# Performance work log

Measured on AMD Instinct MI355X. Metric: run time of the kernel, lower is better.

The kernel has to match this reference:

```python
import jax, jax.numpy as jnp
import numpy as np

N, E, F, HID, HEADS, G = 20000, 320000, 64, 64, 4, 64
HC = HEADS * HID  # 256
NHID, NOUT = 256, 128
INV_SQRT2 = 0.7071067811865476


def _gat(x, src, dst, W, a_s, a_d, bias):
    # GATConv (v1), eval mode (no dropout); src/dst already include self-loops (PyG default)
    H, C = a_s.shape
    h = (x @ W).reshape(-1, H, C)  # [N,H,C]
    al_s = jnp.einsum('nhc,hc->nh', h, a_s)
    al_d = jnp.einsum('nhc,hc->nh', h, a_d)
    e = jax.nn.leaky_relu(al_s[src] + al_d[dst], 0.2)  # [Etot,H]
    m = jax.ops.segment_max(e, dst, num_segments=N)
    ex = jnp.exp(e - m[dst])
    den = jax.ops.segment_sum(ex, dst, num_segments=N)
    coef = ex / den[dst]  # softmax over incoming edges per target node
    out = jax.ops.segment_sum(h[src] * coef[:, :, None], dst, num_segments=N)
    return out.reshape(-1, H * C) + bias


def _bn(h, g, b):
    # BatchNorm1d, training-mode stats (biased var), eps=1e-5
    mu = h.mean(axis=0)
    var = h.var(axis=0)
    return g * (h - mu) * jax.lax.rsqrt(var + 1e-5) + b


def _block(x, src, dst, W1, a1s, a1d, b1, g1, be1, W2, a2s, a2d, b2, g2, be2, Wr, br, Wf, bf):
    h = jax.nn.relu(_bn(_gat(x, src, dst, W1, a1s, a1d, b1), g1, be1))
    h = jax.nn.relu(_bn(_gat(h, src, dst, W2, a2s, a2d, b2), g2, be2))
    res = x @ Wr + br
    return ((h + res) * INV_SQRT2) @ Wf + bf


def setup_inputs():
    ks = iter(jax.random.split(jax.random.key(0), 64))
    def rn(shape, scale=0.05):
        return jax.random.normal(next(ks), shape, dtype=jnp.float32) * scale
    inp = {}
    inp['x'] = jax.random.normal(next(ks), (N, F), dtype=jnp.float32)
    inp['edge_index'] = jax.random.randint(next(ks), (2, E), 0, N, dtype=jnp.int32)
    inp['batch'] = jnp.sort(jax.random.randint(next(ks), (N,), 0, G, dtype=jnp.int32))
    for b, cin in enumerate([F, HID]):
        p = 'b%d_' % b
        inp[p + 'W1'] = rn((cin, HC)); inp[p + 'a1s'] = rn((HEADS, HID)); inp[p + 'a1d'] = rn((HEADS, HID))
        inp[p + 'b1'] = jnp.zeros((HC,), jnp.float32)
        inp[p + 'g1'] = jnp.ones((HC,), jnp.float32); inp[p + 'be1'] = jnp.zeros((HC,), jnp.float32)
        inp[p + 'W2'] = rn((HC, HC)); inp[p + 'a2s'] = rn((1, HC)); inp[p + 'a2d'] = rn((1, HC))
        inp[p + 'b2'] = jnp.zeros((HC,), jnp.float32)
        inp[p + 'g2'] = jnp.ones((HC,), jnp.float32); inp[p + 'be2'] = jnp.zeros((HC,), jnp.float32)
        inp[p + 'Wr'] = rn((cin, HC)); inp[p + 'br'] = jnp.zeros((HC,), jnp.float32)
        inp[p + 'Wf'] = rn((HC, HID)); inp[p + 'bf'] = jnp.zeros((HID,), jnp.float32)
    inp['Wh1'] = rn((HID, NHID)); inp['bh1'] = jnp.zeros((NHID,), jnp.float32)
    inp['Wh2'] = rn((NHID, NOUT)); inp['bh2'] = jnp.zeros((NOUT,), jnp.float32)
    return inp


def reference(x, edge_index, batch,
              b0_W1, b0_a1s, b0_a1d, b0_b1, b0_g1, b0_be1, b0_W2, b0_a2s, b0_a2d, b0_b2, b0_g2, b0_be2, b0_Wr, b0_br, b0_Wf, b0_bf,
              b1_W1, b1_a1s, b1_a1d, b1_b1, b1_g1, b1_be1, b1_W2, b1_a2s, b1_a2d, b1_b2, b1_g2, b1_be2, b1_Wr, b1_br, b1_Wf, b1_bf,
              Wh1, bh1, Wh2, bh2):
    loops = jnp.arange(N, dtype=edge_index.dtype)
    src = jnp.concatenate([edge_index[0], loops])
    dst = jnp.concatenate([edge_index[1], loops])
    x = _block(x, src, dst, b0_W1, b0_a1s, b0_a1d, b0_b1, b0_g1, b0_be1, b0_W2, b0_a2s, b0_a2d, b0_b2, b0_g2, b0_be2, b0_Wr, b0_br, b0_Wf, b0_bf)
    x = _block(x, src, dst, b1_W1, b1_a1s, b1_a1d, b1_b1, b1_g1, b1_be1, b1_W2, b1_a2s, b1_a2d, b1_b2, b1_g2, b1_be2, b1_Wr, b1_br, b1_Wf, b1_bf)
    cnt = jax.ops.segment_sum(jnp.ones((N,), x.dtype), batch, num_segments=G)
    pooled = jax.ops.segment_sum(x, batch, num_segments=G) / jnp.maximum(cnt, 1.0)[:, None]
    h = jax.nn.relu(pooled @ Wh1 + bh1)
    return h @ Wh2 + bh2
```

## Files before the change

### kernel.cpp

```cpp
#include <hip/hip_runtime.h>

#define N_NODES 20000
#define N_EDGES 320000
#define ETOT (N_EDGES + N_NODES)
#define G_GROUPS 64


__global__ __launch_bounds__(256) void k_hist(const int* __restrict__ ei, int* __restrict__ counts) {
    int e = blockIdx.x * 256 + threadIdx.x;
    if (e >= ETOT) return;
    int dst = (e < N_EDGES) ? ei[N_EDGES + e] : (e - N_EDGES);
    atomicAdd(&counts[dst], 1);
}

__global__ __launch_bounds__(1024) void k_scan(const int* __restrict__ counts, int* __restrict__ offs,
                                               int* __restrict__ cursor) {
    __shared__ int sdata[1024];
    const int t = threadIdx.x;
    const int chunk = (N_NODES + 1023) / 1024;
    int base = t * chunk;
    int s = 0;
    for (int i = 0; i < chunk; i++) { int idx = base + i; if (idx < N_NODES) s += counts[idx]; }
    sdata[t] = s;
    __syncthreads();
    for (int off = 1; off < 1024; off <<= 1) {
        int v = (t >= off) ? sdata[t - off] : 0;
        __syncthreads();
        sdata[t] += v;
        __syncthreads();
    }
    int prefix = (t == 0) ? 0 : sdata[t - 1];
    for (int i = 0; i < chunk; i++) {
        int idx = base + i;
        if (idx < N_NODES) {
            int cv = counts[idx];
            offs[idx] = prefix;
            cursor[idx] = prefix;
            prefix += cv;
        }
    }
    if (t == 1023) offs[N_NODES] = sdata[1023];
}

__global__ __launch_bounds__(256) void k_scatter(const int* __restrict__ ei, int* __restrict__ cursor,
                                                 int* __restrict__ csr_src, int* __restrict__ csr_dst) {
    int e = blockIdx.x * 256 + threadIdx.x;
    if (e >= ETOT) return;
    int src = (e < N_EDGES) ? ei[e] : (e - N_EDGES);
    int dst = (e < N_EDGES) ? ei[N_EDGES + e] : (e - N_EDGES);
    int p = atomicAdd(&cursor[dst], 1);
    csr_src[p] = src;
    csr_dst[p] = dst;
}


template <int H>
__global__ __launch_bounds__(256) void k_edgew(const int* __restrict__ csr_src, const int* __restrict__ csr_dst,
                                               const float* __restrict__ alS, const float* __restrict__ alD,
                                               float* __restrict__ wex) {
    int p = blockIdx.x * 256 + threadIdx.x;
    if (p >= ETOT) return;
    int s = csr_src[p], d = csr_dst[p];
    if (H == 4) {
        float4 a = *(const float4*)(alS + s * 4);
        float4 b = *(const float4*)(alD + d * 4);
        float4 v = {a.x + b.x, a.y + b.y, a.z + b.z, a.w + b.w};
        v.x = (v.x > 0.f) ? v.x : 0.2f * v.x;
        v.y = (v.y > 0.f) ? v.y : 0.2f * v.y;
        v.z = (v.z > 0.f) ? v.z : 0.2f * v.z;
        v.w = (v.w > 0.f) ? v.w : 0.2f * v.w;
        float4 w = {__expf(v.x), __expf(v.y), __expf(v.z), __expf(v.w)};
        *(float4*)(wex + p * 4) = w;
    } else {
        float v = alS[s] + alD[d];
        v = (v > 0.f) ? v : 0.2f * v;
        wex[p] = __expf(v);
    }
}


__global__ __launch_bounds__(256) void k_gemm64_dual(const float* __restrict__ x, const float* __restrict__ W1,
                                                     const float* __restrict__ Wr, const float* __restrict__ br,
                                                     const float* __restrict__ a_s, const float* __restrict__ a_d,
                                                     float* __restrict__ h, float* __restrict__ res,
                                                     float* __restrict__ alS, float* __restrict__ alD) {
    const int rb = blockIdx.x >> 2, cs = blockIdx.x & 3;
    const int row0 = rb * 64;
    const int nrows = min(64, N_NODES - row0);
    const int t = threadIdx.x;
    __shared__ float xs[32 * 68];
    __shared__ float b1s[32 * 64];
    __shared__ float brs[32 * 64];
    const int lane = t & 63;
    const int c0 = (t & 15) * 4;
    const int r0 = (t >> 4) * 4;
    float acc1[4][4] = {}, acc2[4][4] = {};
    for (int k0 = 0; k0 < 64; k0 += 32) {
        if (k0) __syncthreads();
        {
            int kk = (t & 7) * 4;
            int r = t >> 3;
            #pragma unroll
            for (int pass = 0; pass < 2; pass++, r += 32) {
                float4 v = {0.f, 0.f, 0.f, 0.f};
                if (r < nrows) v = *(const float4*)(x + (row0 + r) * 64 + k0 + kk);
                xs[(kk + 0) * 68 + r] = v.x;
                xs[(kk + 1) * 68 + r] = v.y;
                xs[(kk + 2) * 68 + r] = v.z;
                xs[(kk + 3) * 68 + r] = v.w;
            }
        }
        {
            int cc = (t & 15) * 4;
            int k = t >> 4;
            #pragma unroll
            for (int pass = 0; pass < 2; pass++, k += 16) {
                *(float4*)(b1s + k * 64 + cc) = *(const float4*)(W1 + (k0 + k) * 256 + cs * 64 + cc);
                *(float4*)(brs + k * 64 + cc) = *(const float4*)(Wr + (k0 + k) * 256 + cs * 64 + cc);
            }
        }
        __syncthreads();
        #pragma unroll 8
        for (int k = 0; k < 32; k++) {
            float4 av = *(const float4*)(xs + k * 68 + r0);
            float4 b1 = *(const float4*)(b1s + k * 64 + c0);
            float4 b2 = *(const float4*)(brs + k * 64 + c0);
            float a[4] = {av.x, av.y, av.z, av.w};
            #pragma unroll
            for (int i = 0; i < 4; i++) {
                acc1[i][0] += a[i] * b1.x; acc1[i][1] += a[i] * b1.y;
                acc1[i][2] += a[i] * b1.z; acc1[i][3] += a[i] * b1.w;
                acc2[i][0] += a[i] * b2.x; acc2[i][1] += a[i] * b2.y;
                acc2[i][2] += a[i] * b2.z; acc2[i][3] += a[i] * b2.w;
            }
        }
    }
    const int gcol = cs * 64 + c0;
    float4 bv = *(const float4*)(br + gcol);
    float4 asv = *(const float4*)(a_s + gcol);
    float4 adv = *(const float4*)(a_d + gcol);
    #pragma unroll
    for (int i = 0; i < 4; i++) {
        int gr = row0 + r0 + i;
        bool ok = (r0 + i) < nrows;
        float4 o1 = {acc1[i][0], acc1[i][1], acc1[i][2], acc1[i][3]};
        if (ok) {
            *(float4*)(h + gr * 256 + gcol) = o1;
            float4 o2 = {acc2[i][0] + bv.x, acc2[i][1] + bv.y, acc2[i][2] + bv.z, acc2[i][3] + bv.w};
            *(float4*)(res + gr * 256 + gcol) = o2;
        }
        float ps = o1.x * asv.x + o1.y * asv.y + o1.z * asv.z + o1.w * asv.w;
        float pd = o1.x * adv.x + o1.y * adv.y + o1.z * adv.z + o1.w * adv.w;
        #pragma unroll
        for (int off = 8; off > 0; off >>= 1) {
            ps += __shfl_down(ps, off);
            pd += __shfl_down(pd, off);
        }
        if (((lane & 15) == 0) && ok) {
            alS[gr * 4 + cs] = ps;
            alD[gr * 4 + cs] = pd;
        }
    }
}


__global__ __launch_bounds__(256) void k_alpha(const float* __restrict__ h, const float* __restrict__ a_s,
                                               const float* __restrict__ a_d, float* __restrict__ alS,
                                               float* __restrict__ alD) {
    int node = blockIdx.x * 4 + (threadIdx.x >> 6);
    int lane = threadIdx.x & 63;
    if (node >= N_NODES) return;
    const float4 hv = *(const float4*)(h + node * 256 + lane * 4);
    const float4 as = *(const float4*)(a_s + lane * 4);
    const float4 ad = *(const float4*)(a_d + lane * 4);
    float ps = hv.x * as.x + hv.y * as.y + hv.z * as.z + hv.w * as.w;
    float pd = hv.x * ad.x + hv.y * ad.y + hv.z * ad.z + hv.w * ad.w;
    #pragma unroll
    for (int off = 32; off > 0; off >>= 1) {
        ps += __shfl_down(ps, off);
        pd += __shfl_down(pd, off);
    }
    if (lane == 0) {
        alS[node] = ps;
        alD[node] = pd;
    }
}


template <int H>
__global__ __launch_bounds__(256) void k_agg(const float* __restrict__ h, const float* __restrict__ wex,
                                             const int* __restrict__ offs, const int* __restrict__ csr_src,
                                             const float* __restrict__ bias, float* __restrict__ out) {
    int node = blockIdx.x * 4 + (threadIdx.x >> 6);
    int lane = threadIdx.x & 63;
    if (node >= N_NODES) return;
    const int head = (lane * H) >> 6;
    int e0 = offs[node], e1 = offs[node + 1];
    float den = 0.f, a0 = 0.f, a1 = 0.f, a2 = 0.f, a3 = 0.f;
    int e = e0;
    for (; e + 4 <= e1; e += 4) {
        int s0 = csr_src[e], s1 = csr_src[e + 1], s2 = csr_src[e + 2], s3 = csr_src[e + 3];
        float w0 = wex[(e + 0) * H + head];
        float w1 = wex[(e + 1) * H + head];
        float w2 = wex[(e + 2) * H + head];
        float w3 = wex[(e + 3) * H + head];
        const float4 h0 = *(const float4*)(h + s0 * 256 + lane * 4);
        const float4 h1 = *(const float4*)(h + s1 * 256 + lane * 4);
        const float4 h2 = *(const float4*)(h + s2 * 256 + lane * 4);
        const float4 h3 = *(const float4*)(h + s3 * 256 + lane * 4);
        den += (w0 + w1) + (w2 + w3);
        a0 += w0 * h0.x + w1 * h1.x + w2 * h2.x + w3 * h3.x;
        a1 += w0 * h0.y + w1 * h1.y + w2 * h2.y + w3 * h3.y;
        a2 += w0 * h0.z + w1 * h1.z + w2 * h2.z + w3 * h3.z;
        a3 += w0 * h0.w + w1 * h1.w + w2 * h2.w + w3 * h3.w;
    }
    for (; e < e1; e++) {
        int s = csr_src[e];
        float w = wex[e * H + head];
        const float4 hv = *(const float4*)(h + s * 256 + lane * 4);
        den += w;
        a0 += w * hv.x; a1 += w * hv.y; a2 += w * hv.z; a3 += w * hv.w;
    }
    float inv = 1.f / den;
    const float4 bv = *(const float4*)(bias + lane * 4);
    float4 o = {a0 * inv + bv.x, a1 * inv + bv.y, a2 * inv + bv.z, a3 * inv + bv.w};
    *(float4*)(out + node * 256 + lane * 4) = o;
}


__global__ __launch_bounds__(256) void k_bnstats(const float* __restrict__ x, float* __restrict__ sum,
                                                 float* __restrict__ sumsq) {
    int c = threadIdx.x;
    float s = 0.f, q = 0.f;
    for (int r = blockIdx.x; r < N_NODES; r += gridDim.x) {
        float v = x[r * 256 + c];
        s += v; q += v * v;
    }
    atomicAdd(&sum[c], s);
    atomicAdd(&sumsq[c], q);
}

__global__ __launch_bounds__(256) void k_bnfin(const float* __restrict__ sum, const float* __restrict__ sumsq,
                                               const float* __restrict__ g, const float* __restrict__ be,
                                               float* __restrict__ scale, float* __restrict__ shift) {
    int c = threadIdx.x;
    float mu = sum[c] * (1.f / N_NODES);
    float var = sumsq[c] * (1.f / N_NODES) - mu * mu;
    float sc = g[c] * rsqrtf(var + 1e-5f);
    scale[c] = sc;
    shift[c] = be[c] - mu * sc;
}


__global__ __launch_bounds__(256) void k_gemm256(const float* __restrict__ A, const float* __restrict__ scale,
                                                 const float* __restrict__ shift, const float* __restrict__ B,
                                                 float* __restrict__ C) {
    const int rb = blockIdx.x >> 2, cs = blockIdx.x & 3;
    const int row0 = rb * 64;
    const int col0 = cs * 64;
    const int nrows = min(64, N_NODES - row0);
    const int t = threadIdx.x;
    __shared__ float xs[32 * 68];
    __shared__ float bs[32 * 64];
    __shared__ float scs[256], shs[256];
    scs[t] = scale[t];
    shs[t] = shift[t];
    const int c0 = (t & 15) * 4;
    const int r0 = (t >> 4) * 4;
    float acc[4][4] = {};
    for (int k0 = 0; k0 < 256; k0 += 32) {
        __syncthreads();
        {
            int kk = (t & 7) * 4;
            int r = t >> 3;
            #pragma unroll
            for (int pass = 0; pass < 2; pass++, r += 32) {
                float4 w = {0.f, 0.f, 0.f, 0.f};
                if (r < nrows) {
                    float4 v = *(const float4*)(A + (row0 + r) * 256 + k0 + kk);
                    int c = k0 + kk;
                    w.x = fmaxf(v.x * scs[c + 0] + shs[c + 0], 0.f);
                    w.y = fmaxf(v.y * scs[c + 1] + shs[c + 1], 0.f);
                    w.z = fmaxf(v.z * scs[c + 2] + shs[c + 2], 0.f);
                    w.w = fmaxf(v.w * scs[c + 3] + shs[c + 3], 0.f);
                }
                xs[(kk + 0) * 68 + r] = w.x;
                xs[(kk + 1) * 68 + r] = w.y;
                xs[(kk + 2) * 68 + r] = w.z;
                xs[(kk + 3) * 68 + r] = w.w;
            }
        }
        {
            int cc = (t & 15) * 4;
            int k = t >> 4;
            #pragma unroll
            for (int pass = 0; pass < 2; pass++, k += 16) {
                *(float4*)(bs + k * 64 + cc) = *(const float4*)(B + (k0 + k) * 256 + col0 + cc);
            }
        }
        __syncthreads();
        #pragma unroll 8
        for (int k = 0; k < 32; k++) {
            float4 av = *(const float4*)(xs + k * 68 + r0);
            float4 bv = *(const float4*)(bs + k * 64 + c0);
            float a[4] = {av.x, av.y, av.z, av.w};
            #pragma unroll
            for (int i = 0; i < 4; i++) {
                acc[i][0] += a[i] * bv.x; acc[i][1] += a[i] * bv.y;
                acc[i][2] += a[i] * bv.z; acc[i][3] += a[i] * bv.w;
            }
        }
    }
    #pragma unroll
    for (int i = 0; i < 4; i++) {
        if ((r0 + i) < nrows) {
            int gr = row0 + r0 + i;
            float4 o = {acc[i][0], acc[i][1], acc[i][2], acc[i][3]};
            *(float4*)(C + gr * 256 + col0 + c0) = o;
        }
    }
}


__global__ __launch_bounds__(256) void k_gemm_final(const float* __restrict__ A, const float* __restrict__ scale,
                                                    const float* __restrict__ shift, const float* __restrict__ res,
                                                    const float* __restrict__ B, const float* __restrict__ bias,
                                                    float* __restrict__ y) {
    const int row0 = blockIdx.x * 32;
    const int t = threadIdx.x;
    const float INVS = 0.70710678118654752440f;
    __shared__ float xs[32 * 36];
    __shared__ float bs[32 * 64];
    __shared__ float scs[256], shs[256];
    scs[t] = scale[t];
    shs[t] = shift[t];
    const int c0 = (t & 15) * 4;
    const int r0 = (t >> 4) * 2;
    float acc[2][4] = {};
    for (int k0 = 0; k0 < 256; k0 += 32) {
        __syncthreads();
        {
            int kk = (t & 7) * 4;
            int r = t >> 3;
            int gi = (row0 + r) * 256 + k0 + kk;
            float4 v = *(const float4*)(A + gi);
            float4 rv = *(const float4*)(res + gi);
            int c = k0 + kk;
            xs[(kk + 0) * 36 + r] = (fmaxf(v.x * scs[c + 0] + shs[c + 0], 0.f) + rv.x) * INVS;
            xs[(kk + 1) * 36 + r] = (fmaxf(v.y * scs[c + 1] + shs[c + 1], 0.f) + rv.y) * INVS;
            xs[(kk + 2) * 36 + r] = (fmaxf(v.z * scs[c + 2] + shs[c + 2], 0.f) + rv.z) * INVS;
            xs[(kk + 3) * 36 + r] = (fmaxf(v.w * scs[c + 3] + shs[c + 3], 0.f) + rv.w) * INVS;
        }
        {
            int cc = (t & 15) * 4;
            int k = t >> 4;
            #pragma unroll
            for (int pass = 0; pass < 2; pass++, k += 16) {
                *(float4*)(bs + k * 64 + cc) = *(const float4*)(B + (k0 + k) * 64 + cc);
            }
        }
        __syncthreads();
        #pragma unroll 8
        for (int k = 0; k < 32; k++) {
            float2 av = *(const float2*)(xs + k * 36 + r0);
            float4 bv = *(const float4*)(bs + k * 64 + c0);
            acc[0][0] += av.x * bv.x; acc[0][1] += av.x * bv.y;
            acc[0][2] += av.x * bv.z; acc[0][3] += av.x * bv.w;
            acc[1][0] += av.y * bv.x; acc[1][1] += av.y * bv.y;
            acc[1][2] += av.y * bv.z; acc[1][3] += av.y * bv.w;
        }
    }
    float4 bv = *(const float4*)(bias + c0);
    #pragma unroll
    for (int i = 0; i < 2; i++) {
        int gr = row0 + r0 + i;
        float4 o = {acc[i][0] + bv.x, acc[i][1] + bv.y, acc[i][2] + bv.z, acc[i][3] + bv.w};
        *(float4*)(y + gr * 64 + c0) = o;
    }
}


__global__ __launch_bounds__(256) void k_pool_head(const float* __restrict__ x, const int* __restrict__ batch,
                                                   const float* __restrict__ Wh1, const float* __restrict__ bh1,
                                                   const float* __restrict__ Wh2, const float* __restrict__ bh2,
                                                   float* __restrict__ out) {
    const int g = blockIdx.x;
    const int t = threadIdx.x;
    int lo = 0, hi = N_NODES;
    while (lo < hi) { int mid = (lo + hi) >> 1; if (batch[mid] < g) lo = mid + 1; else hi = mid; }
    int start = lo;
    hi = N_NODES;
    while (lo < hi) { int mid = (lo + hi) >> 1; if (batch[mid] < g + 1) lo = mid + 1; else hi = mid; }
    int end = lo;
    float cnt = (float)(end - start);

    __shared__ float part[256];
    __shared__ float p[64];
    __shared__ float hrow[256];
    const int c = t & 63;
    float s = 0.f;
    for (int r = start + (t >> 6); r < end; r += 4) s += x[r * 64 + c];
    part[t] = s;
    __syncthreads();
    if (t < 64) {
        float v = part[t] + part[t + 64] + part[t + 128] + part[t + 192];
        p[t] = v / fmaxf(cnt, 1.f);
    }
    __syncthreads();
    float a = bh1[t];
    #pragma unroll 8
    for (int k = 0; k < 64; k++) a += p[k] * Wh1[k * 256 + t];
    hrow[t] = fmaxf(a, 0.f);
    __syncthreads();
    if (t < 128) {
        float o = bh2[t];
        #pragma unroll 8
        for (int k = 0; k < 256; k++) o += hrow[k] * Wh2[k * 128 + t];
        out[g * 128 + t] = o;
    }
}


extern "C" void kernel_launch(void* const* d_in, const int* in_sizes, int n_in,
                              void* d_out, int out_size, void* d_ws, size_t ws_size,
                              hipStream_t stream) {
    (void)in_sizes; (void)n_in; (void)out_size; (void)ws_size;
    const float* x0 = (const float*)d_in[0];
    const int* ei = (const int*)d_in[1];
    const int* batch = (const int*)d_in[2];
    const float* Wh1 = (const float*)d_in[35];
    const float* bh1 = (const float*)d_in[36];
    const float* Wh2 = (const float*)d_in[37];
    const float* bh2 = (const float*)d_in[38];

    char* p = (char*)d_ws;
    auto alloc = [&](size_t bytes) -> void* {
        void* r = (void*)p;
        p += (bytes + 255) & ~(size_t)255;
        return r;
    };
    int* counts = (int*)alloc((size_t)N_NODES * 4);
    int* offs = (int*)alloc((size_t)(N_NODES + 1) * 4);
    int* cursor = (int*)alloc((size_t)N_NODES * 4);
    int* csr_src = (int*)alloc((size_t)ETOT * 4);
    int* csr_dst = (int*)alloc((size_t)ETOT * 4);
    float* wex = (float*)alloc((size_t)ETOT * 4 * 4);
    float* alS = (float*)alloc((size_t)N_NODES * 4 * 4);
    float* alD = (float*)alloc((size_t)N_NODES * 4 * 4);
    float* bnsum = (float*)alloc(2048);
    float* bnsq = bnsum + 256;
    float* scaleb = (float*)alloc(1024);
    float* shiftb = (float*)alloc(1024);
    float* hbuf = (float*)alloc((size_t)N_NODES * 256 * 4);
    float* obuf = (float*)alloc((size_t)N_NODES * 256 * 4);
    float* rbuf = (float*)alloc((size_t)N_NODES * 256 * 4);
    float* xout = (float*)alloc((size_t)N_NODES * 64 * 4);

    hipMemsetAsync(counts, 0, (size_t)N_NODES * 4, stream);
    k_hist<<<(ETOT + 255) / 256, 256, 0, stream>>>(ei, counts);
    k_scan<<<1, 1024, 0, stream>>>(counts, offs, cursor);
    k_scatter<<<(ETOT + 255) / 256, 256, 0, stream>>>(ei, cursor, csr_src, csr_dst);

    const int tile_blocks = ((N_NODES + 63) / 64) * 4;
    const int node_blocks = (N_NODES + 3) / 4;
    const int edge_blocks = (ETOT + 255) / 256;
    const int final_blocks = N_NODES / 32;

    auto run_block = [&](const float* xin, int base) {
        const float* W1 = (const float*)d_in[base + 0];
        const float* a1s = (const float*)d_in[base + 1];
        const float* a1d = (const float*)d_in[base + 2];
        const float* b1 = (const float*)d_in[base + 3];
        const float* g1 = (const float*)d_in[base + 4];
        const float* be1 = (const float*)d_in[base + 5];
        const float* W2 = (const float*)d_in[base + 6];
        const float* a2s = (const float*)d_in[base + 7];
        const float* a2d = (const float*)d_in[base + 8];
        const float* b2 = (const float*)d_in[base + 9];
        const float* g2 = (const float*)d_in[base + 10];
        const float* be2 = (const float*)d_in[base + 11];
        const float* Wr = (const float*)d_in[base + 12];
        const float* br = (const float*)d_in[base + 13];
        const float* Wf = (const float*)d_in[base + 14];
        const float* bf = (const float*)d_in[base + 15];

        k_gemm64_dual<<<tile_blocks, 256, 0, stream>>>(xin, W1, Wr, br, a1s, a1d, hbuf, rbuf, alS, alD);
        k_edgew<4><<<edge_blocks, 256, 0, stream>>>(csr_src, csr_dst, alS, alD, wex);
        k_agg<4><<<node_blocks, 256, 0, stream>>>(hbuf, wex, offs, csr_src, b1, obuf);
        hipMemsetAsync(bnsum, 0, 2048, stream);
        k_bnstats<<<256, 256, 0, stream>>>(obuf, bnsum, bnsq);
        k_bnfin<<<1, 256, 0, stream>>>(bnsum, bnsq, g1, be1, scaleb, shiftb);
        k_gemm256<<<tile_blocks, 256, 0, stream>>>(obuf, scaleb, shiftb, W2, hbuf);
        k_alpha<<<node_blocks, 256, 0, stream>>>(hbuf, a2s, a2d, alS, alD);
        k_edgew<1><<<edge_blocks, 256, 0, stream>>>(csr_src, csr_dst, alS, alD, wex);
        k_agg<1><<<node_blocks, 256, 0, stream>>>(hbuf, wex, offs, csr_src, b2, obuf);
        hipMemsetAsync(bnsum, 0, 2048, stream);
        k_bnstats<<<256, 256, 0, stream>>>(obuf, bnsum, bnsq);
        k_bnfin<<<1, 256, 0, stream>>>(bnsum, bnsq, g2, be2, scaleb, shiftb);
        k_gemm_final<<<final_blocks, 256, 0, stream>>>(obuf, scaleb, shiftb, rbuf, Wf, bf, xout);
    };

    run_block(x0, 3);
    run_block(xout, 19);

    k_pool_head<<<G_GROUPS, 256, 0, stream>>>(xout, batch, Wh1, bh1, Wh2, bh2, (float*)d_out);
}
```

Baseline: 730.9 us.

## Enlarge gemm256 row tile to 128 and remap shared-memory staging for bank conflicts

The 256-wide GEMM now computes 128-row tiles with 8x4 accumulators per thread, halving the number of blocks and reloading each W2 column tile half as often. The A-tile staging loops in all three GEMMs are remapped so consecutive lanes write consecutive rows of the transposed shared tile, which cuts LDS bank conflicts on the transpose stores. In exchange the gemm256 kernel uses more registers and LDS, and its grid shrinks to about 628 blocks, which could lower occupancy.

```diff
diff --git a/kernel.cpp b/kernel.cpp
--- a/kernel.cpp
+++ b/kernel.cpp
@@ -94,20 +94,21 @@
     const int lane = t & 63;
     const int c0 = (t & 15) * 4;
     const int r0 = (t >> 4) * 4;
+    const int rl = (t & 15) | ((t >> 6) << 4);
+    const int c4 = (t >> 4) & 3;
     float acc1[4][4] = {}, acc2[4][4] = {};
     for (int k0 = 0; k0 < 64; k0 += 32) {
         if (k0) __syncthreads();
         {
-            int kk = (t & 7) * 4;
-            int r = t >> 3;
-            #pragma unroll
-            for (int pass = 0; pass < 2; pass++, r += 32) {
+            #pragma unroll
+            for (int jj = 0; jj < 2; jj++) {
+                int cc = c4 + 4 * jj;
                 float4 v = {0.f, 0.f, 0.f, 0.f};
-                if (r < nrows) v = *(const float4*)(x + (row0 + r) * 64 + k0 + kk);
-                xs[(kk + 0) * 68 + r] = v.x;
-                xs[(kk + 1) * 68 + r] = v.y;
-                xs[(kk + 2) * 68 + r] = v.z;
-                xs[(kk + 3) * 68 + r] = v.w;
+                if (rl < nrows) v = *(const float4*)(x + (row0 + rl) * 64 + k0 + cc * 4);
+                xs[(cc * 4 + 0) * 68 + rl] = v.x;
+                xs[(cc * 4 + 1) * 68 + rl] = v.y;
+                xs[(cc * 4 + 2) * 68 + rl] = v.z;
+                xs[(cc * 4 + 3) * 68 + rl] = v.w;
             }
         }
         {
@@ -256,63 +257,67 @@
                                                  const float* __restrict__ shift, const float* __restrict__ B,
                                                  float* __restrict__ C) {
     const int rb = blockIdx.x >> 2, cs = blockIdx.x & 3;
-    const int row0 = rb * 64;
+    const int row0 = rb * 128;
     const int col0 = cs * 64;
-    const int nrows = min(64, N_NODES - row0);
+    const int nrows = min(128, N_NODES - row0);
     const int t = threadIdx.x;
-    __shared__ float xs[32 * 68];
+    __shared__ float xs[32 * 132];
     __shared__ float bs[32 * 64];
     __shared__ float scs[256], shs[256];
     scs[t] = scale[t];
     shs[t] = shift[t];
+    const int rl = (t & 15) | ((t >> 6) << 4);
+    const int c4 = (t >> 4) & 3;
     const int c0 = (t & 15) * 4;
-    const int r0 = (t >> 4) * 4;
-    float acc[4][4] = {};
+    const int r0 = (t >> 4) * 8;
+    float acc[8][4] = {};
     for (int k0 = 0; k0 < 256; k0 += 32) {
         __syncthreads();
-        {
-            int kk = (t & 7) * 4;
-            int r = t >> 3;
-            #pragma unroll
-            for (int pass = 0; pass < 2; pass++, r += 32) {
+        #pragma unroll
+        for (int i = 0; i < 2; i++) {
+            int r = rl + 64 * i;
+            #pragma unroll
+            for (int jj = 0; jj < 2; jj++) {
+                int cc = c4 + 4 * jj;
+                int kcol = k0 + cc * 4;
                 float4 w = {0.f, 0.f, 0.f, 0.f};
                 if (r < nrows) {
-                    float4 v = *(const float4*)(A + (row0 + r) * 256 + k0 + kk);
-                    int c = k0 + kk;
-                    w.x = fmaxf(v.x * scs[c + 0] + shs[c + 0], 0.f);
-                    w.y = fmaxf(v.y * scs[c + 1] + shs[c + 1], 0.f);
-                    w.z = fmaxf(v.z * scs[c + 2] + shs[c + 2], 0.f);
-                    w.w = fmaxf(v.w * scs[c + 3] + shs[c + 3], 0.f);
+                    float4 v = *(const float4*)(A + (row0 + r) * 256 + kcol);
+                    w.x = fmaxf(v.x * scs[kcol + 0] + shs[kcol + 0], 0.f);
+                    w.y = fmaxf(v.y * scs[kcol + 1] + shs[kcol + 1], 0.f);
+                    w.z = fmaxf(v.z * scs[kcol + 2] + shs[kcol + 2], 0.f);
+                    w.w = fmaxf(v.w * scs[kcol + 3] + shs[kcol + 3], 0.f);
                 }
-                xs[(kk + 0) * 68 + r] = w.x;
-                xs[(kk + 1) * 68 + r] = w.y;
-                xs[(kk + 2) * 68 + r] = w.z;
-                xs[(kk + 3) * 68 + r] = w.w;
+                xs[(cc * 4 + 0) * 132 + r] = w.x;
+                xs[(cc * 4 + 1) * 132 + r] = w.y;
+                xs[(cc * 4 + 2) * 132 + r] = w.z;
+                xs[(cc * 4 + 3) * 132 + r] = w.w;
             }
         }
         {
-            int cc = (t & 15) * 4;
-            int k = t >> 4;
-            #pragma unroll
-            for (int pass = 0; pass < 2; pass++, k += 16) {
-                *(float4*)(bs + k * 64 + cc) = *(const float4*)(B + (k0 + k) * 256 + col0 + cc);
+            int ccB = (t & 15) * 4;
+            int kB = t >> 4;
+            #pragma unroll
+            for (int pass = 0; pass < 2; pass++, kB += 16) {
+                *(float4*)(bs + kB * 64 + ccB) = *(const float4*)(B + (k0 + kB) * 256 + col0 + ccB);
             }
         }
         __syncthreads();
         #pragma unroll 8
         for (int k = 0; k < 32; k++) {
-            float4 av = *(const float4*)(xs + k * 68 + r0);
+            float4 a0 = *(const float4*)(xs + k * 132 + r0);
+            float4 a1 = *(const float4*)(xs + k * 132 + r0 + 4);
             float4 bv = *(const float4*)(bs + k * 64 + c0);
-            float a[4] = {av.x, av.y, av.z, av.w};
-            #pragma unroll
-            for (int i = 0; i < 4; i++) {
+            float a[8] = {a0.x, a0.y, a0.z, a0.w, a1.x, a1.y, a1.z, a1.w};
+            #pragma unroll
+            for (int i = 0; i < 8; i++) {
                 acc[i][0] += a[i] * bv.x; acc[i][1] += a[i] * bv.y;
                 acc[i][2] += a[i] * bv.z; acc[i][3] += a[i] * bv.w;
             }
         }
     }
     #pragma unroll
-    for (int i = 0; i < 4; i++) {
+    for (int i = 0; i < 8; i++) {
         if ((r0 + i) < nrows) {
             int gr = row0 + r0 + i;
             float4 o = {acc[i][0], acc[i][1], acc[i][2], acc[i][3]};
@@ -334,22 +339,22 @@
     __shared__ float scs[256], shs[256];
     scs[t] = scale[t];
     shs[t] = shift[t];
+    const int rf = (t & 15) | ((t >> 7) << 4);
+    const int cf = (t >> 4) & 7;
     const int c0 = (t & 15) * 4;
     const int r0 = (t >> 4) * 2;
     float acc[2][4] = {};
     for (int k0 = 0; k0 < 256; k0 += 32) {
         __syncthreads();
         {
-            int kk = (t & 7) * 4;
-            int r = t >> 3;
-            int gi = (row0 + r) * 256 + k0 + kk;
+            int kcol = k0 + cf * 4;
+            int gi = (row0 + rf) * 256 + kcol;
             float4 v = *(const float4*)(A + gi);
             float4 rv = *(const float4*)(res + gi);
-            int c = k0 + kk;
-            xs[(kk + 0) * 36 + r] = (fmaxf(v.x * scs[c + 0] + shs[c + 0], 0.f) + rv.x) * INVS;
-            xs[(kk + 1) * 36 + r] = (fmaxf(v.y * scs[c + 1] + shs[c + 1], 0.f) + rv.y) * INVS;
-            xs[(kk + 2) * 36 + r] = (fmaxf(v.z * scs[c + 2] + shs[c + 2], 0.f) + rv.z) * INVS;
-            xs[(kk + 3) * 36 + r] = (fmaxf(v.w * scs[c + 3] + shs[c + 3], 0.f) + rv.w) * INVS;
+            xs[(cf * 4 + 0) * 36 + rf] = (fmaxf(v.x * scs[kcol + 0] + shs[kcol + 0], 0.f) + rv.x) * INVS;
+            xs[(cf * 4 + 1) * 36 + rf] = (fmaxf(v.y * scs[kcol + 1] + shs[kcol + 1], 0.f) + rv.y) * INVS;
+            xs[(cf * 4 + 2) * 36 + rf] = (fmaxf(v.z * scs[kcol + 2] + shs[kcol + 2], 0.f) + rv.z) * INVS;
+            xs[(cf * 4 + 3) * 36 + rf] = (fmaxf(v.w * scs[kcol + 3] + shs[kcol + 3], 0.f) + rv.w) * INVS;
         }
         {
             int cc = (t & 15) * 4;
@@ -461,7 +466,8 @@
     k_scan<<<1, 1024, 0, stream>>>(counts, offs, cursor);
     k_scatter<<<(ETOT + 255) / 256, 256, 0, stream>>>(ei, cursor, csr_src, csr_dst);
 
-    const int tile_blocks = ((N_NODES + 63) / 64) * 4;
+    const int tile64_blocks = ((N_NODES + 63) / 64) * 4;
+    const int tile128_blocks = ((N_NODES + 127) / 128) * 4;
     const int node_blocks = (N_NODES + 3) / 4;
     const int edge_blocks = (ETOT + 255) / 256;
     const int final_blocks = N_NODES / 32;
@@ -484,13 +490,13 @@
         const float* Wf = (const float*)d_in[base + 14];
         const float* bf = (const float*)d_in[base + 15];
 
-        k_gemm64_dual<<<tile_blocks, 256, 0, stream>>>(xin, W1, Wr, br, a1s, a1d, hbuf, rbuf, alS, alD);
+        k_gemm64_dual<<<tile64_blocks, 256, 0, stream>>>(xin, W1, Wr, br, a1s, a1d, hbuf, rbuf, alS, alD);
         k_edgew<4><<<edge_blocks, 256, 0, stream>>>(csr_src, csr_dst, alS, alD, wex);
         k_agg<4><<<node_blocks, 256, 0, stream>>>(hbuf, wex, offs, csr_src, b1, obuf);
         hipMemsetAsync(bnsum, 0, 2048, stream);
         k_bnstats<<<256, 256, 0, stream>>>(obuf, bnsum, bnsq);
         k_bnfin<<<1, 256, 0, stream>>>(bnsum, bnsq, g1, be1, scaleb, shiftb);
-        k_gemm256<<<tile_blocks, 256, 0, stream>>>(obuf, scaleb, shiftb, W2, hbuf);
+        k_gemm256<<<tile128_blocks, 256, 0, stream>>>(obuf, scaleb, shiftb, W2, hbuf);
         k_alpha<<<node_blocks, 256, 0, stream>>>(hbuf, a2s, a2d, alS, alD);
         k_edgew<1><<<edge_blocks, 256, 0, stream>>>(csr_src, csr_dst, alS, alD, wex);
         k_agg<1><<<node_blocks, 256, 0, stream>>>(hbuf, wex, offs, csr_src, b2, obuf);
```

Result: no change. 738.7 us (+1.1%).
